# Kernel optimization log

Hardware: AMD Instinct MI355X
Metric: run time of the kernel (lower is better)

Reference implementation:

```python
import jax, jax.numpy as jnp
import numpy as np
import math

HID = 2048
NH = 8
KVH = 1
HD = 256
REP = NH // KVH
THETA = 10000.0
B, S = 2, 2048
NEG = -1e9  # additive mask value for disallowed positions


def setup_inputs() -> dict:
    key = jax.random.key(0)
    ks = jax.random.split(key, 6)
    x = jax.random.normal(ks[0], (B, S, HID), dtype=jnp.float32)
    # causal additive mask [B,1,S,S]
    causal = jnp.tril(jnp.ones((S, S), dtype=bool))
    attn_mask = jnp.where(causal, 0.0, NEG).astype(jnp.float32)[None, None]
    attn_mask = jnp.broadcast_to(attn_mask, (B, 1, S, S))
    pos_ids = jnp.broadcast_to(jnp.arange(S, dtype=jnp.int64 if jax.config.jax_enable_x64 else jnp.int32), (B, S))
    sc = 0.02
    wq = jax.random.normal(ks[1], (HID, NH * HD), dtype=jnp.float32) * sc
    wk = jax.random.normal(ks[2], (HID, KVH * HD), dtype=jnp.float32) * sc
    wv = jax.random.normal(ks[3], (HID, KVH * HD), dtype=jnp.float32) * sc
    wo = jax.random.normal(ks[4], (NH * HD, HID), dtype=jnp.float32) * sc
    return {"x": x, "attn_mask": attn_mask, "pos_ids": pos_ids,
            "wq": wq, "wk": wk, "wv": wv, "wo": wo}


def _rotate_half(t):
    h = t.shape[-1] // 2
    return jnp.concatenate([-t[..., h:], t[..., :h]], axis=-1)


def _rope_cos_sin(pos_ids, dtype):
    inv_freq = 1.0 / (THETA ** (jnp.arange(0, HD, 2, dtype=jnp.float32) / HD))  # [HD/2]
    freqs = pos_ids.astype(jnp.float32)[:, :, None] * inv_freq[None, None, :]  # [B,S,HD/2]
    emb = jnp.concatenate([freqs, freqs], axis=-1)                              # [B,S,HD]
    # unsqueeze head dim -> [B,1,S,HD]
    return jnp.cos(emb)[:, None].astype(dtype), jnp.sin(emb)[:, None].astype(dtype)


def reference(x, attn_mask, pos_ids, wq, wk, wv, wo):
    b, s, _ = x.shape
    q = (x @ wq).reshape(b, s, NH, HD).transpose(0, 2, 1, 3)    # [B,NH,S,HD]
    k = (x @ wk).reshape(b, s, KVH, HD).transpose(0, 2, 1, 3)   # [B,KVH,S,HD]
    v = (x @ wv).reshape(b, s, KVH, HD).transpose(0, 2, 1, 3)   # [B,KVH,S,HD]
    cos, sin = _rope_cos_sin(pos_ids, q.dtype)
    q = q * cos + _rotate_half(q) * sin
    k = k * cos + _rotate_half(k) * sin
    # GQA: group query heads over shared KV head instead of materializing repeat_kv
    qg = q.reshape(b, KVH, REP, s, HD)
    scores = jnp.einsum('bgrqd,bgkd->bgrqk', qg, k) / math.sqrt(HD)  # [B,KVH,REP,S,S]
    scores = scores.reshape(b, NH, s, s) + attn_mask
    attn = jax.nn.softmax(scores.astype(jnp.float32), axis=-1).astype(q.dtype)  # [B,NH,S,S]
    # dropout p=0.0 -> identity
    pg = attn.reshape(b, KVH, REP, s, s)
    out = jnp.einsum('bgrqk,bgkd->bgrqd', pg, v).reshape(b, NH, s, HD)
    out = out.transpose(0, 2, 1, 3).reshape(b, s, NH * HD) @ wo  # [B,S,HID]
    return out, attn
```

## Files before the change

kernel.cpp:

```cpp
#include <hip/hip_runtime.h>
#include <cstdint>
#include <cmath>

#define HID_ 2048
#define NH_ 8
#define HD_ 256
#define B_ 2
#define S_ 2048
#define BS_ (B_*S_)
#define QKVW_ 2560

typedef short short8 __attribute__((ext_vector_type(8)));
typedef float floatx4 __attribute__((ext_vector_type(4)));

static __device__ __forceinline__ unsigned short f2bf(float f) {
  union { float f; unsigned u; } v; v.f = f;
  return (unsigned short)((v.u + 0x7FFFu + ((v.u >> 16) & 1u)) >> 16);
}
static __device__ __forceinline__ float bf2f(unsigned short h) {
  union { unsigned u; float f; } v; v.u = ((unsigned)h) << 16;
  return v.f;
}

static __device__ __forceinline__ void gload_lds16(const void* g, void* l) {
  __builtin_amdgcn_global_load_lds(
      (const __attribute__((address_space(1))) unsigned int*)g,
      (__attribute__((address_space(3))) unsigned int*)l, 16, 0, 0);
}


__global__ void cast_f32_bf16_k(const float* __restrict__ in, unsigned short* __restrict__ out, long n) {
  long i = ((long)blockIdx.x * blockDim.x + threadIdx.x) * 4;
  if (i >= n) return;
  float4 v = *reinterpret_cast<const float4*>(in + i);
  ushort4 o; o.x = f2bf(v.x); o.y = f2bf(v.y); o.z = f2bf(v.z); o.w = f2bf(v.w);
  *reinterpret_cast<ushort4*>(out + i) = o;
}

__global__ void transpose_f2b_k(const float* __restrict__ in, unsigned short* __restrict__ out, int R, int C) {
  __shared__ float tile[32][33];
  int c0 = blockIdx.x * 32, r0 = blockIdx.y * 32;
  int tx = threadIdx.x, ty = threadIdx.y;
  #pragma unroll
  for (int i = 0; i < 4; i++)
    tile[ty + i*8][tx] = in[(long)(r0 + ty + i*8) * C + c0 + tx];
  __syncthreads();
  #pragma unroll
  for (int i = 0; i < 4; i++)
    out[(long)(c0 + ty + i*8) * R + r0 + tx] = f2bf(tile[tx][ty + i*8]);
}

__global__ void transpose_strided_k(const unsigned short* __restrict__ in, unsigned short* __restrict__ out,
                                    int ld_in, int ld_out, long in_bs, long out_bs) {
  __shared__ unsigned short tile[32][33];
  in += (long)blockIdx.z * in_bs; out += (long)blockIdx.z * out_bs;
  int c0 = blockIdx.x * 32, r0 = blockIdx.y * 32;
  int tx = threadIdx.x, ty = threadIdx.y;
  #pragma unroll
  for (int i = 0; i < 4; i++)
    tile[ty + i*8][tx] = in[(long)(r0 + ty + i*8) * ld_in + c0 + tx];
  __syncthreads();
  #pragma unroll
  for (int i = 0; i < 4; i++)
    out[(long)(c0 + ty + i*8) * ld_out + r0 + tx] = tile[tx][ty + i*8];
}

__global__ void rope_k(unsigned short* __restrict__ qk, const int* __restrict__ pos_ids,
                       int heads, int row_stride, long total) {
  long idx = (long)blockIdx.x * blockDim.x + threadIdx.x;
  if (idx >= total) return;
  int per_row = heads * (HD_/2);
  int r  = (int)(idx / per_row);
  int rem = (int)(idx % per_row);
  int h = rem / (HD_/2);
  int i = rem % (HD_/2);
  float posf = (float)pos_ids[r];
  float freq = expf(-(float)i * (logf(10000.0f) / 128.0f));
  float ang = posf * freq;
  float c = cosf(ang), s = sinf(ang);
  unsigned short* p = qk + (long)r * row_stride + (long)h * HD_;
  float a = bf2f(p[i]), b = bf2f(p[i + 128]);
  p[i]       = f2bf(a * c - b * s);
  p[i + 128] = f2bf(b * c + a * s);
}

template<int EPI>
__global__ __launch_bounds__(256)
void gemm_bt_k(const void* __restrict__ Av, const unsigned short* __restrict__ Bt,
               void* __restrict__ Cv, int K, long lda, long ldb, long ldc) {
  __shared__ unsigned short Al[128 * 32];
  __shared__ unsigned short Bl[128 * 32];

  int tid = threadIdx.x;
  int lane = tid & 63, wave = tid >> 6;
  int bm = blockIdx.y * 128, bn = blockIdx.x * 128;

  const unsigned short* Abase = (const unsigned short*)Av + (long)bm * lda;
  const unsigned short* Bbase = Bt + (long)bn * ldb;

  floatx4 zero = {0.f, 0.f, 0.f, 0.f};
  floatx4 acc[4][4];
  #pragma unroll
  for (int i = 0; i < 4; i++)
    #pragma unroll
    for (int j = 0; j < 4; j++) acc[i][j] = zero;

  const int wm = (wave >> 1) * 64, wn = (wave & 1) * 64;
  const int lr = lane & 15, lq = lane >> 4;

  for (int k0 = 0; k0 < K; k0 += 32) {
    #pragma unroll
    for (int c = 0; c < 2; c++) {
      int e = c * 2048 + tid * 8;
      int row = e >> 5, col = e & 31;
      gload_lds16(Abase + (long)row * lda + k0 + col, (char*)Al + c * 4096 + wave * 1024);
    }
    #pragma unroll
    for (int c = 0; c < 2; c++) {
      int e = c * 2048 + tid * 8;
      int row = e >> 5, col = e & 31;
      gload_lds16(Bbase + (long)row * ldb + k0 + col, (char*)Bl + c * 4096 + wave * 1024);
    }
    __syncthreads();

    short8 af[4], bfr[4];
    #pragma unroll
    for (int i = 0; i < 4; i++)
      af[i] = *reinterpret_cast<const short8*>(&Al[(wm + i*16 + lr) * 32 + lq * 8]);
    #pragma unroll
    for (int j = 0; j < 4; j++)
      bfr[j] = *reinterpret_cast<const short8*>(&Bl[(wn + j*16 + lr) * 32 + lq * 8]);
    #pragma unroll
    for (int i = 0; i < 4; i++)
      #pragma unroll
      for (int j = 0; j < 4; j++)
        acc[i][j] = __builtin_amdgcn_mfma_f32_16x16x32_bf16(af[i], bfr[j], acc[i][j], 0, 0, 0);
    __syncthreads();
  }

  if (EPI == 0) {
    unsigned short* C = (unsigned short*)Cv;
    #pragma unroll
    for (int i = 0; i < 4; i++)
      #pragma unroll
      for (int r = 0; r < 4; r++) {
        int row = bm + wm + i*16 + lq*4 + r;
        #pragma unroll
        for (int j = 0; j < 4; j++) {
          int col = bn + wn + j*16 + lr;
          C[(long)row * ldc + col] = f2bf(acc[i][j][r]);
        }
      }
  } else {
    float* C = (float*)Cv;
    #pragma unroll
    for (int i = 0; i < 4; i++)
      #pragma unroll
      for (int r = 0; r < 4; r++) {
        int row = bm + wm + i*16 + lq*4 + r;
        #pragma unroll
        for (int j = 0; j < 4; j++) {
          int col = bn + wn + j*16 + lr;
          C[(long)row * ldc + col] = acc[i][j][r];
        }
      }
  }
}

__global__ __launch_bounds__(256, 2)
void attn_fused_k(const unsigned short* __restrict__ qkv, const unsigned short* __restrict__ v_t,
                  float* __restrict__ attn, unsigned short* __restrict__ o_bf) {
  int z = blockIdx.x;
  int b = z >> 3, h = z & 7;
  int t = 31 - blockIdx.y;
  int bm = t * 64;
  int nkt = t / 2 + 1;

  const unsigned short* Qg = qkv + (long)b * S_ * QKVW_ + (long)h * HD_;
  const unsigned short* Kg = qkv + (long)b * S_ * QKVW_ + 2048;
  const unsigned short* Vt = v_t + (long)b * HD_ * S_;
  float* Az = attn + (long)z * S_ * S_;

  __shared__ unsigned short Kb[2][128 * 64];
  __shared__ unsigned short Vb[2][128 * 64];

  int tid = threadIdx.x;
  int lane = tid & 63, wave = tid >> 6;
  int lr = lane & 15, lq = lane >> 4;

  {
    int ce = nkt * 128;
    int perrow = (S_ - ce) >> 2;
    float4 zf = {0.f, 0.f, 0.f, 0.f};
    for (int i = tid; i < 64 * perrow; i += 256) {
      int r = i / perrow, c = i - r * perrow;
      *reinterpret_cast<float4*>(Az + (long)(bm + r) * S_ + ce + c * 4) = zf;
    }
  }

  short8 aq[8];
  {
    const unsigned short* qrow = Qg + (long)(bm + wave*16 + lr) * QKVW_;
    #pragma unroll
    for (int f = 0; f < 8; f++)
      aq[f] = *reinterpret_cast<const short8*>(qrow + f*32 + lq*8);
  }

  auto stageK = [&](int kt_, int c_) {
    char* dst = (char*)Kb[(kt_ + c_) & 1];
    const unsigned short* src = Kg + (long)(kt_ * 128) * QKVW_ + c_ * 64;
    #pragma unroll
    for (int cc = 0; cc < 4; cc++) {
      int q = cc * 256 + tid;
      int row = q >> 3, g = q & 7;
      gload_lds16(src + (long)row * QKVW_ + ((g ^ (row & 7)) << 3),
                  dst + cc * 4096 + wave * 1024);
    }
  };
  auto stageV = [&](int kt_, int p_) {
    int dh = p_ & 1, sh = p_ >> 1;
    char* dst = (char*)Vb[p_ & 1];
    const unsigned short* src = Vt + (long)(dh * 128) * S_ + kt_ * 128 + sh * 64;
    #pragma unroll
    for (int cc = 0; cc < 4; cc++) {
      int q = cc * 256 + tid;
      int row = q >> 3, g = q & 7;
      gload_lds16(src + (long)row * S_ + ((g ^ (row & 7)) << 3),
                  dst + cc * 4096 + wave * 1024);
    }
  };

  floatx4 zero = {0.f, 0.f, 0.f, 0.f};
  float rsum[4] = {0.f, 0.f, 0.f, 0.f};

  stageK(0, 0);
  __syncthreads();
  for (int kt = 0; kt < nkt; kt++) {
    floatx4 sacc[8];
    #pragma unroll
    for (int j = 0; j < 8; j++) sacc[j] = zero;
    #pragma unroll
    for (int c = 0; c < 4; c++) {
      if (c < 3) stageK(kt, c + 1);
      const unsigned short* Kc = Kb[(kt + c) & 1];
      #pragma unroll
      for (int kk = 0; kk < 2; kk++) {
        #pragma unroll
        for (int j = 0; j < 8; j++) {
          int R = j*16 + lr, G = kk*4 + lq;
          short8 bk = *reinterpret_cast<const short8*>(&Kc[R*64 + ((G ^ (R & 7)) << 3)]);
          sacc[j] = __builtin_amdgcn_mfma_f32_16x16x32_bf16(aq[c*2 + kk], bk, sacc[j], 0, 0, 0);
        }
      }
      __syncthreads();
    }
    if (kt + 1 < nkt) stageK(kt + 1, 0);
    #pragma unroll
    for (int j = 0; j < 8; j++)
      #pragma unroll
      for (int r = 0; r < 4; r++) {
        int row_l = wave*16 + lq*4 + r;
        int col_g = kt*128 + j*16 + lr;
        rsum[r] += (col_g <= bm + row_l) ? __expf(sacc[j][r] * 0.0625f) : 0.f;
      }
    __syncthreads();
  }

  float inv[4];
  #pragma unroll
  for (int r = 0; r < 4; r++) {
    float s = rsum[r];
    #pragma unroll
    for (int o = 1; o < 16; o <<= 1) s += __shfl_xor(s, o, 64);
    inv[r] = 1.0f / s;
  }

  floatx4 oacc[16];
  #pragma unroll
  for (int j = 0; j < 16; j++) oacc[j] = zero;

  stageK(0, 0);
  __syncthreads();

  for (int kt = 0; kt < nkt; kt++) {
    int pb = kt & 1;
    floatx4 sacc[8];
    #pragma unroll
    for (int j = 0; j < 8; j++) sacc[j] = zero;

    #pragma unroll
    for (int c = 0; c < 4; c++) {
      if (c < 3) stageK(kt, c + 1);
      if (c == 2) stageV(kt, 0);
      if (c == 3) stageV(kt, 1);
      const unsigned short* Kc = Kb[(kt + c) & 1];
      #pragma unroll
      for (int kk = 0; kk < 2; kk++) {
        #pragma unroll
        for (int j = 0; j < 8; j++) {
          int R = j*16 + lr, G = kk*4 + lq;
          short8 bk = *reinterpret_cast<const short8*>(&Kc[R*64 + ((G ^ (R & 7)) << 3)]);
          sacc[j] = __builtin_amdgcn_mfma_f32_16x16x32_bf16(aq[c*2 + kk], bk, sacc[j], 0, 0, 0);
        }
      }
      __syncthreads();
    }

    unsigned short* Pl = Kb[pb];
    #pragma unroll
    for (int j = 0; j < 8; j++) {
      float v[4];
      #pragma unroll
      for (int r = 0; r < 4; r++) {
        int row_l = wave*16 + lq*4 + r;
        int col_g = kt*128 + j*16 + lr;
        float pv = (col_g <= bm + row_l) ? __expf(sacc[j][r] * 0.0625f) * inv[r] : 0.f;
        v[r] = pv;
        int Gw = j*2 + (lr >> 3);
        Pl[row_l*128 + ((Gw ^ (row_l & 7)) << 3) + (lr & 7)] = f2bf(pv);
      }
      float w[4];
      #pragma unroll
      for (int r = 0; r < 4; r++) w[r] = __shfl_xor(v[r], 1, 64);
      int colb = kt*128 + j*16 + (lr & ~1);
      if (!(lr & 1)) {
        #pragma unroll
        for (int r = 0; r < 2; r++) {
          int row = bm + wave*16 + lq*4 + r;
          float2 st; st.x = v[r]; st.y = w[r];
          *reinterpret_cast<float2*>(Az + (long)row * S_ + colb) = st;
        }
      } else {
        #pragma unroll
        for (int r = 2; r < 4; r++) {
          int row = bm + wave*16 + lq*4 + r;
          float2 st; st.x = w[r]; st.y = v[r];
          *reinterpret_cast<float2*>(Az + (long)row * S_ + colb) = st;
        }
      }
    }

    #pragma unroll
    for (int p = 0; p < 4; p++) {
      if (p == 0 && kt + 1 < nkt) stageK(kt + 1, 0);
      if (p == 1) stageV(kt, 2);
      if (p == 2) stageV(kt, 3);
      int dh = p & 1, sh = p >> 1;
      const unsigned short* Vc = Vb[p & 1];
      short8 ap[2];
      #pragma unroll
      for (int kk = 0; kk < 2; kk++) {
        int R = wave*16 + lr, G = sh*8 + kk*4 + lq;
        ap[kk] = *reinterpret_cast<const short8*>(&Pl[R*128 + ((G ^ (R & 7)) << 3)]);
      }
      #pragma unroll
      for (int kk = 0; kk < 2; kk++) {
        #pragma unroll
        for (int j2 = 0; j2 < 8; j2++) {
          int R = j2*16 + lr, G = kk*4 + lq;
          short8 bv = *reinterpret_cast<const short8*>(&Vc[R*64 + ((G ^ (R & 7)) << 3)]);
          oacc[dh*8 + j2] = __builtin_amdgcn_mfma_f32_16x16x32_bf16(ap[kk], bv, oacc[dh*8 + j2], 0, 0, 0);
        }
      }
      __syncthreads();
    }
  }

  unsigned short* C = o_bf + (long)b * S_ * HID_ + (long)h * HD_;
  #pragma unroll
  for (int dh = 0; dh < 2; dh++)
    #pragma unroll
    for (int j2 = 0; j2 < 8; j2++)
      #pragma unroll
      for (int r = 0; r < 4; r++) {
        int row = bm + wave*16 + lq*4 + r;
        int col = dh*128 + j2*16 + lr;
        C[(long)row * HID_ + col] = f2bf(oacc[dh*8 + j2][r]);
      }
}


extern "C" void kernel_launch(void* const* d_in, const int* in_sizes, int n_in,
                              void* d_out, int out_size, void* d_ws, size_t ws_size,
                              hipStream_t stream) {
  (void)in_sizes; (void)n_in; (void)out_size; (void)ws_size;
  const float* x   = (const float*)d_in[0];
  const int*   pos = (const int*)d_in[2];
  const float* wq  = (const float*)d_in[3];
  const float* wk  = (const float*)d_in[4];
  const float* wv  = (const float*)d_in[5];
  const float* wo  = (const float*)d_in[6];
  float* out  = (float*)d_out;
  float* attn = out + (long)B_ * S_ * HID_;

  char* p = (char*)d_ws;
  auto take = [&](size_t n) { char* r = p; p += (n + 255) & ~(size_t)255; return r; };
  unsigned short* x_bf   = (unsigned short*)take((size_t)BS_ * HID_ * 2);
  unsigned short* wqkv_t = (unsigned short*)take((size_t)QKVW_ * HID_ * 2);
  unsigned short* wo_t   = (unsigned short*)take((size_t)HID_ * HID_ * 2);
  unsigned short* qkv    = (unsigned short*)take((size_t)BS_ * QKVW_ * 2);
  unsigned short* v_t    = (unsigned short*)take((size_t)B_ * HD_ * S_ * 2);
  unsigned short* o_bf   = (unsigned short*)take((size_t)BS_ * HID_ * 2);

  dim3 tb(32, 8);

  cast_f32_bf16_k<<<(BS_ * HID_) / 1024, 256, 0, stream>>>(x, x_bf, (long)BS_ * HID_);

  transpose_f2b_k<<<dim3(HID_/32, HID_/32), tb, 0, stream>>>(wq, wqkv_t, HID_, HID_);
  transpose_f2b_k<<<dim3(HD_/32,  HID_/32), tb, 0, stream>>>(wk, wqkv_t + (size_t)2048 * HID_, HID_, HD_);
  transpose_f2b_k<<<dim3(HD_/32,  HID_/32), tb, 0, stream>>>(wv, wqkv_t + (size_t)2304 * HID_, HID_, HD_);
  transpose_f2b_k<<<dim3(HID_/32, HID_/32), tb, 0, stream>>>(wo, wo_t, HID_, HID_);

  gemm_bt_k<0><<<dim3(QKVW_/128, BS_/128), 256, 0, stream>>>(
      x_bf, wqkv_t, qkv, HID_, HID_, HID_, QKVW_);

  rope_k<<<(BS_ * NH_ * (HD_/2)) / 256, 256, 0, stream>>>(
      qkv, pos, NH_, QKVW_, (long)BS_ * NH_ * (HD_/2));
  rope_k<<<(BS_ * (HD_/2)) / 256, 256, 0, stream>>>(
      qkv + 2048, pos, 1, QKVW_, (long)BS_ * (HD_/2));

  transpose_strided_k<<<dim3(HD_/32, S_/32, B_), tb, 0, stream>>>(
      qkv + 2304, v_t, QKVW_, S_, (long)S_ * QKVW_, (long)HD_ * S_);

  attn_fused_k<<<dim3(B_ * NH_, S_/64), 256, 0, stream>>>(qkv, v_t, attn, o_bf);

  gemm_bt_k<1><<<dim3(HID_/128, BS_/128), 256, 0, stream>>>(
      o_bf, wo_t, out, HID_, HID_, HID_, HID_);
}
```

Baseline: 649.1 us.

## Split attention into single-wave blocks loading K/V directly from global memory

Each attention block is reduced from four waves covering 64 query rows to one wave covering 16 rows, and the grid grows fourfold. K and V tiles are read straight from global memory into registers for the MFMA operands instead of being staged through double-buffered LDS with barriers. Only the P tile stays in LDS. This removes the __syncthreads and staging overhead, but every wave now re-fetches K/V on its own and depends on L1/L2 hits rather than shared LDS reuse.

New measurement: 940.0 us. +44.8%, slower.

```diff
diff --git a/kernel.cpp b/kernel.cpp
--- a/kernel.cpp
+++ b/kernel.cpp
@@ -167,13 +167,16 @@
   }
 }
 
-__global__ __launch_bounds__(256, 2)
+__global__ __launch_bounds__(64, 2)
 void attn_fused_k(const unsigned short* __restrict__ qkv, const unsigned short* __restrict__ v_t,
                   float* __restrict__ attn, unsigned short* __restrict__ o_bf) {
   int z = blockIdx.x;
   int b = z >> 3, h = z & 7;
-  int t = 31 - blockIdx.y;
+  int yy = blockIdx.y;
+  int t = 31 - (yy >> 2);
+  int sub = yy & 3;
   int bm = t * 64;
+  int qr0 = bm + sub * 16;
   int nkt = t / 2 + 1;
 
   const unsigned short* Qg = qkv + (long)b * S_ * QKVW_ + (long)h * HD_;
@@ -181,89 +184,56 @@
   const unsigned short* Vt = v_t + (long)b * HD_ * S_;
   float* Az = attn + (long)z * S_ * S_;
 
-  __shared__ unsigned short Kb[2][128 * 64];
-  __shared__ unsigned short Vb[2][128 * 64];
-
-  int tid = threadIdx.x;
-  int lane = tid & 63, wave = tid >> 6;
+  __shared__ unsigned short Pl[16 * 128];
+
+  int lane = threadIdx.x & 63;
   int lr = lane & 15, lq = lane >> 4;
 
   {
     int ce = nkt * 128;
     int perrow = (S_ - ce) >> 2;
     float4 zf = {0.f, 0.f, 0.f, 0.f};
-    for (int i = tid; i < 64 * perrow; i += 256) {
+    for (int i = lane; i < 16 * perrow; i += 64) {
       int r = i / perrow, c = i - r * perrow;
-      *reinterpret_cast<float4*>(Az + (long)(bm + r) * S_ + ce + c * 4) = zf;
+      *reinterpret_cast<float4*>(Az + (long)(qr0 + r) * S_ + ce + c * 4) = zf;
     }
   }
 
   short8 aq[8];
   {
-    const unsigned short* qrow = Qg + (long)(bm + wave*16 + lr) * QKVW_;
+    const unsigned short* qrow = Qg + (long)(qr0 + lr) * QKVW_;
     #pragma unroll
     for (int f = 0; f < 8; f++)
       aq[f] = *reinterpret_cast<const short8*>(qrow + f*32 + lq*8);
   }
 
-  auto stageK = [&](int kt_, int c_) {
-    char* dst = (char*)Kb[(kt_ + c_) & 1];
-    const unsigned short* src = Kg + (long)(kt_ * 128) * QKVW_ + c_ * 64;
-    #pragma unroll
-    for (int cc = 0; cc < 4; cc++) {
-      int q = cc * 256 + tid;
-      int row = q >> 3, g = q & 7;
-      gload_lds16(src + (long)row * QKVW_ + ((g ^ (row & 7)) << 3),
-                  dst + cc * 4096 + wave * 1024);
-    }
-  };
-  auto stageV = [&](int kt_, int p_) {
-    int dh = p_ & 1, sh = p_ >> 1;
-    char* dst = (char*)Vb[p_ & 1];
-    const unsigned short* src = Vt + (long)(dh * 128) * S_ + kt_ * 128 + sh * 64;
-    #pragma unroll
-    for (int cc = 0; cc < 4; cc++) {
-      int q = cc * 256 + tid;
-      int row = q >> 3, g = q & 7;
-      gload_lds16(src + (long)row * S_ + ((g ^ (row & 7)) << 3),
-                  dst + cc * 4096 + wave * 1024);
-    }
-  };
+  const unsigned short* Kln = Kg + (long)lr * QKVW_ + lq * 8;
+  const unsigned short* Vln = Vt + (long)lr * S_ + lq * 8;
 
   floatx4 zero = {0.f, 0.f, 0.f, 0.f};
   float rsum[4] = {0.f, 0.f, 0.f, 0.f};
 
-  stageK(0, 0);
-  __syncthreads();
   for (int kt = 0; kt < nkt; kt++) {
     floatx4 sacc[8];
     #pragma unroll
     for (int j = 0; j < 8; j++) sacc[j] = zero;
-    #pragma unroll
-    for (int c = 0; c < 4; c++) {
-      if (c < 3) stageK(kt, c + 1);
-      const unsigned short* Kc = Kb[(kt + c) & 1];
-      #pragma unroll
-      for (int kk = 0; kk < 2; kk++) {
-        #pragma unroll
-        for (int j = 0; j < 8; j++) {
-          int R = j*16 + lr, G = kk*4 + lq;
-          short8 bk = *reinterpret_cast<const short8*>(&Kc[R*64 + ((G ^ (R & 7)) << 3)]);
-          sacc[j] = __builtin_amdgcn_mfma_f32_16x16x32_bf16(aq[c*2 + kk], bk, sacc[j], 0, 0, 0);
-        }
-      }
-      __syncthreads();
-    }
-    if (kt + 1 < nkt) stageK(kt + 1, 0);
+    const unsigned short* Kt = Kln + (long)(kt * 128) * QKVW_;
+    #pragma unroll
+    for (int f = 0; f < 8; f++) {
+      #pragma unroll
+      for (int j = 0; j < 8; j++) {
+        short8 bk = *reinterpret_cast<const short8*>(Kt + (long)(j * 16) * QKVW_ + f * 32);
+        sacc[j] = __builtin_amdgcn_mfma_f32_16x16x32_bf16(aq[f], bk, sacc[j], 0, 0, 0);
+      }
+    }
     #pragma unroll
     for (int j = 0; j < 8; j++)
       #pragma unroll
       for (int r = 0; r < 4; r++) {
-        int row_l = wave*16 + lq*4 + r;
+        int row_l = lq*4 + r;
         int col_g = kt*128 + j*16 + lr;
-        rsum[r] += (col_g <= bm + row_l) ? __expf(sacc[j][r] * 0.0625f) : 0.f;
-      }
-    __syncthreads();
+        rsum[r] += (col_g <= qr0 + row_l) ? __expf(sacc[j][r] * 0.0625f) : 0.f;
+      }
   }
 
   float inv[4];
@@ -279,42 +249,28 @@
   #pragma unroll
   for (int j = 0; j < 16; j++) oacc[j] = zero;
 
-  stageK(0, 0);
-  __syncthreads();
-
   for (int kt = 0; kt < nkt; kt++) {
-    int pb = kt & 1;
     floatx4 sacc[8];
     #pragma unroll
     for (int j = 0; j < 8; j++) sacc[j] = zero;
-
-    #pragma unroll
-    for (int c = 0; c < 4; c++) {
-      if (c < 3) stageK(kt, c + 1);
-      if (c == 2) stageV(kt, 0);
-      if (c == 3) stageV(kt, 1);
-      const unsigned short* Kc = Kb[(kt + c) & 1];
-      #pragma unroll
-      for (int kk = 0; kk < 2; kk++) {
-        #pragma unroll
-        for (int j = 0; j < 8; j++) {
-          int R = j*16 + lr, G = kk*4 + lq;
-          short8 bk = *reinterpret_cast<const short8*>(&Kc[R*64 + ((G ^ (R & 7)) << 3)]);
-          sacc[j] = __builtin_amdgcn_mfma_f32_16x16x32_bf16(aq[c*2 + kk], bk, sacc[j], 0, 0, 0);
-        }
-      }
-      __syncthreads();
-    }
-
-    unsigned short* Pl = Kb[pb];
+    const unsigned short* Kt = Kln + (long)(kt * 128) * QKVW_;
+    #pragma unroll
+    for (int f = 0; f < 8; f++) {
+      #pragma unroll
+      for (int j = 0; j < 8; j++) {
+        short8 bk = *reinterpret_cast<const short8*>(Kt + (long)(j * 16) * QKVW_ + f * 32);
+        sacc[j] = __builtin_amdgcn_mfma_f32_16x16x32_bf16(aq[f], bk, sacc[j], 0, 0, 0);
+      }
+    }
+
     #pragma unroll
     for (int j = 0; j < 8; j++) {
       float v[4];
       #pragma unroll
       for (int r = 0; r < 4; r++) {
-        int row_l = wave*16 + lq*4 + r;
+        int row_l = lq*4 + r;
         int col_g = kt*128 + j*16 + lr;
-        float pv = (col_g <= bm + row_l) ? __expf(sacc[j][r] * 0.0625f) * inv[r] : 0.f;
+        float pv = (col_g <= qr0 + row_l) ? __expf(sacc[j][r] * 0.0625f) * inv[r] : 0.f;
         v[r] = pv;
         int Gw = j*2 + (lr >> 3);
         Pl[row_l*128 + ((Gw ^ (row_l & 7)) << 3) + (lr & 7)] = f2bf(pv);
@@ -326,57 +282,40 @@
       if (!(lr & 1)) {
         #pragma unroll
         for (int r = 0; r < 2; r++) {
-          int row = bm + wave*16 + lq*4 + r;
           float2 st; st.x = v[r]; st.y = w[r];
-          *reinterpret_cast<float2*>(Az + (long)row * S_ + colb) = st;
+          *reinterpret_cast<float2*>(Az + (long)(qr0 + lq*4 + r) * S_ + colb) = st;
         }
       } else {
         #pragma unroll
         for (int r = 2; r < 4; r++) {
-          int row = bm + wave*16 + lq*4 + r;
           float2 st; st.x = w[r]; st.y = v[r];
-          *reinterpret_cast<float2*>(Az + (long)row * S_ + colb) = st;
+          *reinterpret_cast<float2*>(Az + (long)(qr0 + lq*4 + r) * S_ + colb) = st;
         }
       }
     }
 
     #pragma unroll
-    for (int p = 0; p < 4; p++) {
-      if (p == 0 && kt + 1 < nkt) stageK(kt + 1, 0);
-      if (p == 1) stageV(kt, 2);
-      if (p == 2) stageV(kt, 3);
-      int dh = p & 1, sh = p >> 1;
-      const unsigned short* Vc = Vb[p & 1];
-      short8 ap[2];
-      #pragma unroll
-      for (int kk = 0; kk < 2; kk++) {
-        int R = wave*16 + lr, G = sh*8 + kk*4 + lq;
-        ap[kk] = *reinterpret_cast<const short8*>(&Pl[R*128 + ((G ^ (R & 7)) << 3)]);
-      }
-      #pragma unroll
-      for (int kk = 0; kk < 2; kk++) {
-        #pragma unroll
-        for (int j2 = 0; j2 < 8; j2++) {
-          int R = j2*16 + lr, G = kk*4 + lq;
-          short8 bv = *reinterpret_cast<const short8*>(&Vc[R*64 + ((G ^ (R & 7)) << 3)]);
-          oacc[dh*8 + j2] = __builtin_amdgcn_mfma_f32_16x16x32_bf16(ap[kk], bv, oacc[dh*8 + j2], 0, 0, 0);
-        }
-      }
-      __syncthreads();
+    for (int ks = 0; ks < 4; ks++) {
+      int Gp = ks*4 + lq;
+      short8 ap = *reinterpret_cast<const short8*>(&Pl[lr*128 + ((Gp ^ (lr & 7)) << 3)]);
+      const unsigned short* Vk = Vln + kt*128 + ks*32;
+      #pragma unroll
+      for (int dj = 0; dj < 16; dj++) {
+        short8 bv = *reinterpret_cast<const short8*>(Vk + (long)(dj * 16) * S_);
+        oacc[dj] = __builtin_amdgcn_mfma_f32_16x16x32_bf16(ap, bv, oacc[dj], 0, 0, 0);
+      }
     }
   }
 
   unsigned short* C = o_bf + (long)b * S_ * HID_ + (long)h * HD_;
   #pragma unroll
-  for (int dh = 0; dh < 2; dh++)
-    #pragma unroll
-    for (int j2 = 0; j2 < 8; j2++)
-      #pragma unroll
-      for (int r = 0; r < 4; r++) {
-        int row = bm + wave*16 + lq*4 + r;
-        int col = dh*128 + j2*16 + lr;
-        C[(long)row * HID_ + col] = f2bf(oacc[dh*8 + j2][r]);
-      }
+  for (int dj = 0; dj < 16; dj++)
+    #pragma unroll
+    for (int r = 0; r < 4; r++) {
+      int row = qr0 + lq*4 + r;
+      int col = dj*16 + lr;
+      C[(long)row * HID_ + col] = f2bf(oacc[dj][r]);
+    }
 }
 
 
@@ -422,7 +361,7 @@
   transpose_strided_k<<<dim3(HD_/32, S_/32, B_), tb, 0, stream>>>(
       qkv + 2304, v_t, QKVW_, S_, (long)S_ * QKVW_, (long)HD_ * S_);
 
-  attn_fused_k<<<dim3(B_ * NH_, S_/64), 256, 0, stream>>>(qkv, v_t, attn, o_bf);
+  attn_fused_k<<<dim3(B_ * NH_, 128), 64, 0, stream>>>(qkv, v_t, attn, o_bf);
 
   gemm_bt_k<1><<<dim3(HID_/128, BS_/128), 256, 0, stream>>>(
       o_bf, wo_t, out, HID_, HID_, HID_, HID_);
```

## Pair complementary causal query tiles per 512-thread attention block sharing K/V staging

Applied to the files above, without the earlier changes.

Each attention block now handles two 64-row query tiles (t and 31-t) with 8 waves, so causal work per block is balanced and K/V tiles staged in shared memory serve both tiles. K staging uses 128-wide head-dim chunks and P gets its own shared buffer. Waves whose tile has finished its key tiles stay idle but still join barriers, and the larger shared memory footprint and block size may lower occupancy.

Result: faster. 632.1 us (-2.6%).

```diff
diff --git a/kernel.cpp b/kernel.cpp
--- a/kernel.cpp
+++ b/kernel.cpp
@@ -167,66 +167,72 @@
   }
 }
 
-__global__ __launch_bounds__(256, 2)
+__global__ __launch_bounds__(512, 2)
 void attn_fused_k(const unsigned short* __restrict__ qkv, const unsigned short* __restrict__ v_t,
                   float* __restrict__ attn, unsigned short* __restrict__ o_bf) {
   int z = blockIdx.x;
   int b = z >> 3, h = z & 7;
-  int t = 31 - blockIdx.y;
-  int bm = t * 64;
-  int nkt = t / 2 + 1;
+  int pp = blockIdx.y;
+  int ta = 31 - pp, tb = pp;
+  int nkt_a = ta / 2 + 1;
+  int nkt_b = tb / 2 + 1;
 
   const unsigned short* Qg = qkv + (long)b * S_ * QKVW_ + (long)h * HD_;
   const unsigned short* Kg = qkv + (long)b * S_ * QKVW_ + 2048;
   const unsigned short* Vt = v_t + (long)b * HD_ * S_;
   float* Az = attn + (long)z * S_ * S_;
 
-  __shared__ unsigned short Kb[2][128 * 64];
+  __shared__ unsigned short Kb[2][128 * 128];
   __shared__ unsigned short Vb[2][128 * 64];
+  __shared__ unsigned short Pb[128 * 128];
 
   int tid = threadIdx.x;
   int lane = tid & 63, wave = tid >> 6;
   int lr = lane & 15, lq = lane >> 4;
+  int wt = wave >> 2;
+  int bm = (wt ? tb : ta) * 64;
+  int qr0 = bm + (wave & 3) * 16;
+  int my_nkt = wt ? nkt_b : nkt_a;
 
   {
-    int ce = nkt * 128;
+    int ce = my_nkt * 128;
     int perrow = (S_ - ce) >> 2;
     float4 zf = {0.f, 0.f, 0.f, 0.f};
-    for (int i = tid; i < 64 * perrow; i += 256) {
+    for (int i = lane; i < 16 * perrow; i += 64) {
       int r = i / perrow, c = i - r * perrow;
-      *reinterpret_cast<float4*>(Az + (long)(bm + r) * S_ + ce + c * 4) = zf;
+      *reinterpret_cast<float4*>(Az + (long)(qr0 + r) * S_ + ce + c * 4) = zf;
     }
   }
 
   short8 aq[8];
   {
-    const unsigned short* qrow = Qg + (long)(bm + wave*16 + lr) * QKVW_;
+    const unsigned short* qrow = Qg + (long)(qr0 + lr) * QKVW_;
     #pragma unroll
     for (int f = 0; f < 8; f++)
       aq[f] = *reinterpret_cast<const short8*>(qrow + f*32 + lq*8);
   }
 
   auto stageK = [&](int kt_, int c_) {
-    char* dst = (char*)Kb[(kt_ + c_) & 1];
-    const unsigned short* src = Kg + (long)(kt_ * 128) * QKVW_ + c_ * 64;
+    char* dst = (char*)Kb[c_];
+    const unsigned short* src = Kg + (long)(kt_ * 128) * QKVW_ + c_ * 128;
     #pragma unroll
     for (int cc = 0; cc < 4; cc++) {
-      int q = cc * 256 + tid;
-      int row = q >> 3, g = q & 7;
+      int q = cc * 512 + tid;
+      int row = q >> 4, g = q & 15;
       gload_lds16(src + (long)row * QKVW_ + ((g ^ (row & 7)) << 3),
-                  dst + cc * 4096 + wave * 1024);
+                  dst + cc * 8192 + wave * 1024);
     }
   };
   auto stageV = [&](int kt_, int p_) {
-    int dh = p_ & 1, sh = p_ >> 1;
+    int sh = p_ >> 1, dh = p_ & 1;
     char* dst = (char*)Vb[p_ & 1];
     const unsigned short* src = Vt + (long)(dh * 128) * S_ + kt_ * 128 + sh * 64;
     #pragma unroll
-    for (int cc = 0; cc < 4; cc++) {
-      int q = cc * 256 + tid;
+    for (int cc = 0; cc < 2; cc++) {
+      int q = cc * 512 + tid;
       int row = q >> 3, g = q & 7;
       gload_lds16(src + (long)row * S_ + ((g ^ (row & 7)) << 3),
-                  dst + cc * 4096 + wave * 1024);
+                  dst + cc * 8192 + wave * 1024);
     }
   };
 
@@ -235,148 +241,164 @@
 
   stageK(0, 0);
   __syncthreads();
-  for (int kt = 0; kt < nkt; kt++) {
+  for (int kt = 0; kt < nkt_a; kt++) {
+    bool live = kt < my_nkt;
     floatx4 sacc[8];
     #pragma unroll
     for (int j = 0; j < 8; j++) sacc[j] = zero;
-    #pragma unroll
-    for (int c = 0; c < 4; c++) {
-      if (c < 3) stageK(kt, c + 1);
-      const unsigned short* Kc = Kb[(kt + c) & 1];
-      #pragma unroll
-      for (int kk = 0; kk < 2; kk++) {
+    stageK(kt, 1);
+    if (live) {
+      #pragma unroll
+      for (int kk = 0; kk < 4; kk++)
         #pragma unroll
         for (int j = 0; j < 8; j++) {
           int R = j*16 + lr, G = kk*4 + lq;
-          short8 bk = *reinterpret_cast<const short8*>(&Kc[R*64 + ((G ^ (R & 7)) << 3)]);
-          sacc[j] = __builtin_amdgcn_mfma_f32_16x16x32_bf16(aq[c*2 + kk], bk, sacc[j], 0, 0, 0);
-        }
+          short8 bk = *reinterpret_cast<const short8*>(&Kb[0][R*128 + ((G ^ (R & 7)) << 3)]);
+          sacc[j] = __builtin_amdgcn_mfma_f32_16x16x32_bf16(aq[kk], bk, sacc[j], 0, 0, 0);
+        }
+    }
+    __syncthreads();
+    if (kt + 1 < nkt_a) stageK(kt + 1, 0);
+    if (live) {
+      #pragma unroll
+      for (int kk = 0; kk < 4; kk++)
+        #pragma unroll
+        for (int j = 0; j < 8; j++) {
+          int R = j*16 + lr, G = kk*4 + lq;
+          short8 bk = *reinterpret_cast<const short8*>(&Kb[1][R*128 + ((G ^ (R & 7)) << 3)]);
+          sacc[j] = __builtin_amdgcn_mfma_f32_16x16x32_bf16(aq[4 + kk], bk, sacc[j], 0, 0, 0);
+        }
+      #pragma unroll
+      for (int j = 0; j < 8; j++)
+        #pragma unroll
+        for (int r = 0; r < 4; r++) {
+          int row_l = lq*4 + r;
+          int col_g = kt*128 + j*16 + lr;
+          rsum[r] += (col_g <= qr0 + row_l) ? __expf(sacc[j][r] * 0.0625f) : 0.f;
+        }
+    }
+    __syncthreads();
+  }
+
+  float inv[4];
+  #pragma unroll
+  for (int r = 0; r < 4; r++) {
+    float s = rsum[r];
+    #pragma unroll
+    for (int o = 1; o < 16; o <<= 1) s += __shfl_xor(s, o, 64);
+    inv[r] = 1.0f / s;
+  }
+
+  floatx4 oacc[16];
+  #pragma unroll
+  for (int j = 0; j < 16; j++) oacc[j] = zero;
+
+  stageK(0, 0);
+  __syncthreads();
+
+  for (int kt = 0; kt < nkt_a; kt++) {
+    bool live = kt < my_nkt;
+    floatx4 sacc[8];
+    #pragma unroll
+    for (int j = 0; j < 8; j++) sacc[j] = zero;
+
+    stageK(kt, 1);
+    stageV(kt, 0);
+    if (live) {
+      #pragma unroll
+      for (int kk = 0; kk < 4; kk++)
+        #pragma unroll
+        for (int j = 0; j < 8; j++) {
+          int R = j*16 + lr, G = kk*4 + lq;
+          short8 bk = *reinterpret_cast<const short8*>(&Kb[0][R*128 + ((G ^ (R & 7)) << 3)]);
+          sacc[j] = __builtin_amdgcn_mfma_f32_16x16x32_bf16(aq[kk], bk, sacc[j], 0, 0, 0);
+        }
+    }
+    __syncthreads();
+
+    if (kt + 1 < nkt_a) stageK(kt + 1, 0);
+    stageV(kt, 1);
+    if (live) {
+      #pragma unroll
+      for (int kk = 0; kk < 4; kk++)
+        #pragma unroll
+        for (int j = 0; j < 8; j++) {
+          int R = j*16 + lr, G = kk*4 + lq;
+          short8 bk = *reinterpret_cast<const short8*>(&Kb[1][R*128 + ((G ^ (R & 7)) << 3)]);
+          sacc[j] = __builtin_amdgcn_mfma_f32_16x16x32_bf16(aq[4 + kk], bk, sacc[j], 0, 0, 0);
+        }
+    }
+    __syncthreads();
+
+    if (live) {
+      #pragma unroll
+      for (int j = 0; j < 8; j++) {
+        float v[4];
+        #pragma unroll
+        for (int r = 0; r < 4; r++) {
+          int row_l = lq*4 + r;
+          int col_g = kt*128 + j*16 + lr;
+          float pv = (col_g <= qr0 + row_l) ? __expf(sacc[j][r] * 0.0625f) * inv[r] : 0.f;
+          v[r] = pv;
+          int row_p = wave*16 + row_l;
+          int Gw = j*2 + (lr >> 3);
+          Pb[row_p*128 + ((Gw ^ (row_p & 7)) << 3) + (lr & 7)] = f2bf(pv);
+        }
+        float w[4];
+        #pragma unroll
+        for (int r = 0; r < 4; r++) w[r] = __shfl_xor(v[r], 1, 64);
+        int colb = kt*128 + j*16 + (lr & ~1);
+        if (!(lr & 1)) {
+          #pragma unroll
+          for (int r = 0; r < 2; r++) {
+            float2 st; st.x = v[r]; st.y = w[r];
+            *reinterpret_cast<float2*>(Az + (long)(qr0 + lq*4 + r) * S_ + colb) = st;
+          }
+        } else {
+          #pragma unroll
+          for (int r = 2; r < 4; r++) {
+            float2 st; st.x = w[r]; st.y = v[r];
+            *reinterpret_cast<float2*>(Az + (long)(qr0 + lq*4 + r) * S_ + colb) = st;
+          }
+        }
+      }
+    }
+
+    #pragma unroll
+    for (int p = 0; p < 4; p++) {
+      if (p == 1) stageV(kt, 2);
+      if (p == 2) stageV(kt, 3);
+      if (live) {
+        int sh = p >> 1, dh = p & 1;
+        const unsigned short* Vc = Vb[p & 1];
+        short8 ap[2];
+        #pragma unroll
+        for (int kk = 0; kk < 2; kk++) {
+          int Rp = wave*16 + lr, G = sh*8 + kk*4 + lq;
+          ap[kk] = *reinterpret_cast<const short8*>(&Pb[Rp*128 + ((G ^ (Rp & 7)) << 3)]);
+        }
+        #pragma unroll
+        for (int kk = 0; kk < 2; kk++)
+          #pragma unroll
+          for (int dj = 0; dj < 8; dj++) {
+            int R = dj*16 + lr, G = kk*4 + lq;
+            short8 bv = *reinterpret_cast<const short8*>(&Vc[R*64 + ((G ^ (R & 7)) << 3)]);
+            oacc[dh*8 + dj] = __builtin_amdgcn_mfma_f32_16x16x32_bf16(ap[kk], bv, oacc[dh*8 + dj], 0, 0, 0);
+          }
       }
       __syncthreads();
     }
-    if (kt + 1 < nkt) stageK(kt + 1, 0);
-    #pragma unroll
-    for (int j = 0; j < 8; j++)
-      #pragma unroll
-      for (int r = 0; r < 4; r++) {
-        int row_l = wave*16 + lq*4 + r;
-        int col_g = kt*128 + j*16 + lr;
-        rsum[r] += (col_g <= bm + row_l) ? __expf(sacc[j][r] * 0.0625f) : 0.f;
-      }
-    __syncthreads();
-  }
-
-  float inv[4];
-  #pragma unroll
-  for (int r = 0; r < 4; r++) {
-    float s = rsum[r];
-    #pragma unroll
-    for (int o = 1; o < 16; o <<= 1) s += __shfl_xor(s, o, 64);
-    inv[r] = 1.0f / s;
-  }
-
-  floatx4 oacc[16];
-  #pragma unroll
-  for (int j = 0; j < 16; j++) oacc[j] = zero;
-
-  stageK(0, 0);
-  __syncthreads();
-
-  for (int kt = 0; kt < nkt; kt++) {
-    int pb = kt & 1;
-    floatx4 sacc[8];
-    #pragma unroll
-    for (int j = 0; j < 8; j++) sacc[j] = zero;
-
-    #pragma unroll
-    for (int c = 0; c < 4; c++) {
-      if (c < 3) stageK(kt, c + 1);
-      if (c == 2) stageV(kt, 0);
-      if (c == 3) stageV(kt, 1);
-      const unsigned short* Kc = Kb[(kt + c) & 1];
-      #pragma unroll
-      for (int kk = 0; kk < 2; kk++) {
-        #pragma unroll
-        for (int j = 0; j < 8; j++) {
-          int R = j*16 + lr, G = kk*4 + lq;
-          short8 bk = *reinterpret_cast<const short8*>(&Kc[R*64 + ((G ^ (R & 7)) << 3)]);
-          sacc[j] = __builtin_amdgcn_mfma_f32_16x16x32_bf16(aq[c*2 + kk], bk, sacc[j], 0, 0, 0);
-        }
-      }
-      __syncthreads();
-    }
-
-    unsigned short* Pl = Kb[pb];
-    #pragma unroll
-    for (int j = 0; j < 8; j++) {
-      float v[4];
-      #pragma unroll
-      for (int r = 0; r < 4; r++) {
-        int row_l = wave*16 + lq*4 + r;
-        int col_g = kt*128 + j*16 + lr;
-        float pv = (col_g <= bm + row_l) ? __expf(sacc[j][r] * 0.0625f) * inv[r] : 0.f;
-        v[r] = pv;
-        int Gw = j*2 + (lr >> 3);
-        Pl[row_l*128 + ((Gw ^ (row_l & 7)) << 3) + (lr & 7)] = f2bf(pv);
-      }
-      float w[4];
-      #pragma unroll
-      for (int r = 0; r < 4; r++) w[r] = __shfl_xor(v[r], 1, 64);
-      int colb = kt*128 + j*16 + (lr & ~1);
-      if (!(lr & 1)) {
-        #pragma unroll
-        for (int r = 0; r < 2; r++) {
-          int row = bm + wave*16 + lq*4 + r;
-          float2 st; st.x = v[r]; st.y = w[r];
-          *reinterpret_cast<float2*>(Az + (long)row * S_ + colb) = st;
-        }
-      } else {
-        #pragma unroll
-        for (int r = 2; r < 4; r++) {
-          int row = bm + wave*16 + lq*4 + r;
-          float2 st; st.x = w[r]; st.y = v[r];
-          *reinterpret_cast<float2*>(Az + (long)row * S_ + colb) = st;
-        }
-      }
-    }
-
-    #pragma unroll
-    for (int p = 0; p < 4; p++) {
-      if (p == 0 && kt + 1 < nkt) stageK(kt + 1, 0);
-      if (p == 1) stageV(kt, 2);
-      if (p == 2) stageV(kt, 3);
-      int dh = p & 1, sh = p >> 1;
-      const unsigned short* Vc = Vb[p & 1];
-      short8 ap[2];
-      #pragma unroll
-      for (int kk = 0; kk < 2; kk++) {
-        int R = wave*16 + lr, G = sh*8 + kk*4 + lq;
-        ap[kk] = *reinterpret_cast<const short8*>(&Pl[R*128 + ((G ^ (R & 7)) << 3)]);
-      }
-      #pragma unroll
-      for (int kk = 0; kk < 2; kk++) {
-        #pragma unroll
-        for (int j2 = 0; j2 < 8; j2++) {
-          int R = j2*16 + lr, G = kk*4 + lq;
-          short8 bv = *reinterpret_cast<const short8*>(&Vc[R*64 + ((G ^ (R & 7)) << 3)]);
-          oacc[dh*8 + j2] = __builtin_amdgcn_mfma_f32_16x16x32_bf16(ap[kk], bv, oacc[dh*8 + j2], 0, 0, 0);
-        }
-      }
-      __syncthreads();
-    }
   }
 
   unsigned short* C = o_bf + (long)b * S_ * HID_ + (long)h * HD_;
   #pragma unroll
-  for (int dh = 0; dh < 2; dh++)
-    #pragma unroll
-    for (int j2 = 0; j2 < 8; j2++)
-      #pragma unroll
-      for (int r = 0; r < 4; r++) {
-        int row = bm + wave*16 + lq*4 + r;
-        int col = dh*128 + j2*16 + lr;
-        C[(long)row * HID_ + col] = f2bf(oacc[dh*8 + j2][r]);
-      }
+  for (int j2 = 0; j2 < 16; j2++)
+    #pragma unroll
+    for (int r = 0; r < 4; r++) {
+      int row = qr0 + lq*4 + r;
+      int col = j2*16 + lr;
+      C[(long)row * HID_ + col] = f2bf(oacc[j2][r]);
+    }
 }
 
 
@@ -422,7 +444,7 @@
   transpose_strided_k<<<dim3(HD_/32, S_/32, B_), tb, 0, stream>>>(
       qkv + 2304, v_t, QKVW_, S_, (long)S_ * QKVW_, (long)HD_ * S_);
 
-  attn_fused_k<<<dim3(B_ * NH_, S_/64), 256, 0, stream>>>(qkv, v_t, attn, o_bf);
+  attn_fused_k<<<dim3(B_ * NH_, 16), 512, 0, stream>>>(qkv, v_t, attn, o_bf);
 
   gemm_bt_k<1><<<dim3(HID_/128, BS_/128), 256, 0, stream>>>(
       o_bf, wo_t, out, HID_, HID_, HID_, HID_);
```
